# Optimization experiments

Hardware: AMD Instinct MI355X
Metric: run time of the kernel (lower is better)

The kernel has to match this reference:

```python
import jax, jax.numpy as jnp
import numpy as np

N, K, D, L = 4096, 64, 1024, 16384  # tokens, top-k, d_in, num_latents


def setup_inputs() -> dict:
    key = jax.random.key(0)
    ks = jax.random.split(key, 9)
    x = jax.random.normal(ks[0], (N, D), jnp.float32)
    y = jax.random.normal(ks[1], (N, D), jnp.float32)
    latent_acts = jax.random.uniform(ks[2], (N, K), jnp.float32)  # post-topk acts (nonneg)
    latent_indices = jax.random.randint(ks[3], (N, K), 0, L)
    W_dec = jax.random.normal(ks[4], (L, D), jnp.float32) / np.sqrt(D).astype(np.float32)
    b_dec = jax.random.normal(ks[5], (D,), jnp.float32) * 0.01
    post_enc = jax.random.normal(ks[6], (L,), jnp.float32) * 0.01
    post_enc_scale = 1.0 + 0.1 * jax.random.normal(ks[7], (L,), jnp.float32)
    W_skip = jax.random.normal(ks[8], (D, D), jnp.float32) / np.sqrt(D).astype(np.float32)
    return {
        "x": x, "y": y,
        "latent_acts": latent_acts, "latent_indices": latent_indices,
        "W_dec": W_dec, "b_dec": b_dec,
        "post_enc": post_enc, "post_enc_scale": post_enc_scale,
        "W_skip": W_skip,
    }


def reference(x, y, latent_acts, latent_indices, W_dec, b_dec, post_enc, post_enc_scale, W_skip):
    # current_latent_acts: per-index bias gather + indexed scaling
    acts = (latent_acts + post_enc[latent_indices]) * post_enc_scale[latent_indices]  # [N,K]
    # decode: gather W_dec rows by top-k indices, weighted combine, add decoder bias
    sae_out = jnp.einsum('nk,nkd->nd', acts, W_dec[latent_indices]) + b_dec  # [N,D]
    # skip connection: x @ W_skip.mT
    sae_out = sae_out + x @ W_skip.T
    # FVU loss
    e = y - sae_out
    total_variance = jnp.sum((y - jnp.mean(y, axis=0)) ** 2)
    fvu = jnp.sum(e ** 2) / total_variance
    return sae_out, fvu
```

## Files before the change

kernel.cpp:

```cpp
#include <hip/hip_runtime.h>
#include <hip/hip_bf16.h>
#include <cstdint>

#define N_TOK 4096
#define KTOP  64
#define DIM   1024
#define NLAT  16384
#define NCHUNK 8

typedef __bf16 bf16x8 __attribute__((ext_vector_type(8)));
typedef float  floatx4 __attribute__((ext_vector_type(4)));

#define GLOBAL_AS(p) ((const __attribute__((address_space(1))) void*)(p))
#define LDS_AS(p)    ((__attribute__((address_space(3))) void*)(p))

__device__ inline unsigned short f2bf(float f){
  unsigned int u = __float_as_uint(f);
  unsigned int r = (u + 0x7fffu + ((u >> 16) & 1u)) >> 16;
  return (unsigned short)r;
}
__device__ inline float bflo(unsigned int u){ return __uint_as_float(u << 16); }
__device__ inline float bfhi(unsigned int u){ return __uint_as_float(u & 0xffff0000u); }

__global__ __launch_bounds__(256) void cvt_bf16_kernel(
    const float* __restrict__ in, unsigned short* __restrict__ out, int n4){
  int i = blockIdx.x * blockDim.x + threadIdx.x;
  if (i >= n4) return;
  float4 v = ((const float4*)in)[i];
  ushort4 o;
  o.x = f2bf(v.x); o.y = f2bf(v.y); o.z = f2bf(v.z); o.w = f2bf(v.w);
  ((ushort4*)out)[i] = o;
}

__global__ __launch_bounds__(256) void cvt_wdec_chunked(
    const float* __restrict__ Wd, unsigned short* __restrict__ out){
  const int lat = blockIdx.x;
  const int t   = threadIdx.x;
  float4 v = ((const float4*)(Wd + (size_t)lat * DIM))[t];
  ushort4 o;
  o.x = f2bf(v.x); o.y = f2bf(v.y); o.z = f2bf(v.z); o.w = f2bf(v.w);
  const int chunk = t >> 5;
  const int off   = (t & 31) * 4;
  *(ushort4*)(out + ((size_t)chunk * NLAT + lat) * 128 + off) = o;
}

__global__ __launch_bounds__(256) void skip_gemm(
    const unsigned short* __restrict__ xb,
    const unsigned short* __restrict__ wb,
    const float* __restrict__ b_dec,
    float* __restrict__ out){
  __shared__ unsigned short As[128][32];
  __shared__ unsigned short Bs[128][32];
  const int row0 = blockIdx.x * 128;
  const int col0 = blockIdx.y * 128;
  const int t    = threadIdx.x;
  const int lane = t & 63;
  const int w    = t >> 6;
  const int wr   = (w >> 1) * 64;
  const int wc   = (w & 1) * 64;
  const int lm   = lane & 15;
  const int kq   = lane >> 4;
  const int sr   = t >> 2;
  const int sc   = (t & 3) * 8;

  floatx4 acc[4][4] = {};

  for (int k0 = 0; k0 < DIM; k0 += 32){
    __builtin_amdgcn_global_load_lds(GLOBAL_AS(xb + (size_t)(row0 + sr) * DIM + k0 + sc),
                                     LDS_AS(&As[sr][sc]), 16, 0, 0);
    __builtin_amdgcn_global_load_lds(GLOBAL_AS(xb + (size_t)(row0 + 64 + sr) * DIM + k0 + sc),
                                     LDS_AS(&As[64 + sr][sc]), 16, 0, 0);
    __builtin_amdgcn_global_load_lds(GLOBAL_AS(wb + (size_t)(col0 + sr) * DIM + k0 + sc),
                                     LDS_AS(&Bs[sr][sc]), 16, 0, 0);
    __builtin_amdgcn_global_load_lds(GLOBAL_AS(wb + (size_t)(col0 + 64 + sr) * DIM + k0 + sc),
                                     LDS_AS(&Bs[64 + sr][sc]), 16, 0, 0);
    __syncthreads();
    bf16x8 af[4], bfr[4];
    #pragma unroll
    for (int mi = 0; mi < 4; mi++) af[mi] = *(const bf16x8*)(&As[wr + mi * 16 + lm][kq * 8]);
    #pragma unroll
    for (int ni = 0; ni < 4; ni++) bfr[ni] = *(const bf16x8*)(&Bs[wc + ni * 16 + lm][kq * 8]);
    #pragma unroll
    for (int mi = 0; mi < 4; mi++)
      #pragma unroll
      for (int ni = 0; ni < 4; ni++)
        acc[mi][ni] = __builtin_amdgcn_mfma_f32_16x16x32_bf16(af[mi], bfr[ni], acc[mi][ni], 0, 0, 0);
    __syncthreads();
  }

  const int rq = (lane >> 4) * 4;
  #pragma unroll
  for (int mi = 0; mi < 4; mi++){
    #pragma unroll
    for (int ni = 0; ni < 4; ni++){
      int col = col0 + wc + ni * 16 + lm;
      float bd = b_dec[col];
      #pragma unroll
      for (int r = 0; r < 4; r++){
        int row = row0 + wr + mi * 16 + rq + r;
        out[(size_t)row * DIM + col] = acc[mi][ni][r] + bd;
      }
    }
  }
}

__global__ __launch_bounds__(256) void decode_residual(
    const float* __restrict__ y,
    const float* __restrict__ la,
    const int*   __restrict__ li,
    const unsigned short* __restrict__ Wdc,
    const float* __restrict__ pe,
    const float* __restrict__ pes,
    float* __restrict__ out,
    float* __restrict__ sse){
  const int chunk = blockIdx.x & 7;
  const int tok0  = (blockIdx.x >> 3) * 16;
  const int t  = threadIdx.x;
  const int tl = t >> 4;
  const int cl = t & 15;
  __shared__ float s_act[16][KTOP];
  __shared__ int   s_idx[16][KTOP];
  __shared__ float s_red[4];
  #pragma unroll
  for (int i = 0; i < 4; i++){
    int e = t + i * 256;
    int id = li[(tok0 + (e >> 6)) * KTOP + (e & 63)];
    s_idx[e >> 6][e & 63] = id;
    s_act[e >> 6][e & 63] = (la[(tok0 + (e >> 6)) * KTOP + (e & 63)] + pe[id]) * pes[id];
  }
  __syncthreads();
  const int n = tok0 + tl;
  float* op = out + (size_t)n * DIM + chunk * 128 + cl * 8;
  float4 o0 = ((const float4*)op)[0], o1 = ((const float4*)op)[1];
  float acc[8] = {o0.x, o0.y, o0.z, o0.w, o1.x, o1.y, o1.z, o1.w};
  const unsigned short* Wc = Wdc + (size_t)chunk * NLAT * 128 + cl * 8;
  #pragma unroll 8
  for (int k = 0; k < KTOP; k++){
    const float a = s_act[tl][k];
    const uint4 wv = *(const uint4*)(Wc + (size_t)s_idx[tl][k] * 128);
    acc[0] += a * bflo(wv.x); acc[1] += a * bfhi(wv.x);
    acc[2] += a * bflo(wv.y); acc[3] += a * bfhi(wv.y);
    acc[4] += a * bflo(wv.z); acc[5] += a * bfhi(wv.z);
    acc[6] += a * bflo(wv.w); acc[7] += a * bfhi(wv.w);
  }
  ((float4*)op)[0] = make_float4(acc[0], acc[1], acc[2], acc[3]);
  ((float4*)op)[1] = make_float4(acc[4], acc[5], acc[6], acc[7]);
  const float* yp = y + (size_t)n * DIM + chunk * 128 + cl * 8;
  float4 y0 = ((const float4*)yp)[0], y1 = ((const float4*)yp)[1];
  float e0 = y0.x - acc[0], e1 = y0.y - acc[1], e2 = y0.z - acc[2], e3 = y0.w - acc[3];
  float e4 = y1.x - acc[4], e5 = y1.y - acc[5], e6 = y1.z - acc[6], e7 = y1.w - acc[7];
  float s = e0*e0 + e1*e1 + e2*e2 + e3*e3 + e4*e4 + e5*e5 + e6*e6 + e7*e7;
  #pragma unroll
  for (int off = 32; off > 0; off >>= 1) s += __shfl_down(s, off, 64);
  if ((t & 63) == 0) s_red[t >> 6] = s;
  __syncthreads();
  if (t == 0) atomicAdd(sse, s_red[0] + s_red[1] + s_red[2] + s_red[3]);
}

__global__ __launch_bounds__(256) void ystats(
    const float* __restrict__ y, float* __restrict__ colsum, float* __restrict__ sumsq){
  const int t  = threadIdx.x;
  const int r0 = blockIdx.x * 32;
  float4 cs = {0.f, 0.f, 0.f, 0.f};
  float sq = 0.f;
  for (int r = 0; r < 32; r++){
    float4 v = ((const float4*)(y + (size_t)(r0 + r) * DIM))[t];
    cs.x += v.x; cs.y += v.y; cs.z += v.z; cs.w += v.w;
    sq += v.x*v.x + v.y*v.y + v.z*v.z + v.w*v.w;
  }
  atomicAdd(&colsum[t*4+0], cs.x);
  atomicAdd(&colsum[t*4+1], cs.y);
  atomicAdd(&colsum[t*4+2], cs.z);
  atomicAdd(&colsum[t*4+3], cs.w);
  #pragma unroll
  for (int off = 32; off > 0; off >>= 1) sq += __shfl_down(sq, off, 64);
  __shared__ float s_red[4];
  if ((t & 63) == 0) s_red[t >> 6] = sq;
  __syncthreads();
  if (t == 0) atomicAdd(sumsq, s_red[0] + s_red[1] + s_red[2] + s_red[3]);
}

__global__ __launch_bounds__(256) void fvu_kernel(
    const float* __restrict__ ws, float* __restrict__ fvu_out){
  const int t = threadIdx.x;
  float4 c = ((const float4*)(ws + 4))[t];
  float s = c.x*c.x + c.y*c.y + c.z*c.z + c.w*c.w;
  #pragma unroll
  for (int off = 32; off > 0; off >>= 1) s += __shfl_down(s, off, 64);
  __shared__ float s_red[4];
  if ((t & 63) == 0) s_red[t >> 6] = s;
  __syncthreads();
  if (t == 0){
    float ss = s_red[0] + s_red[1] + s_red[2] + s_red[3];
    float tv = ws[1] - ss / (float)N_TOK;
    fvu_out[0] = ws[0] / tv;
  }
}

extern "C" void kernel_launch(void* const* d_in, const int* in_sizes, int n_in,
                              void* d_out, int out_size, void* d_ws, size_t ws_size,
                              hipStream_t stream){
  const float* x   = (const float*)d_in[0];
  const float* y   = (const float*)d_in[1];
  const float* la  = (const float*)d_in[2];
  const int*   li  = (const int*)d_in[3];
  const float* Wd  = (const float*)d_in[4];
  const float* bd  = (const float*)d_in[5];
  const float* pe  = (const float*)d_in[6];
  const float* pes = (const float*)d_in[7];
  const float* Wsk = (const float*)d_in[8];
  float* out = (float*)d_out;

  float* accs = (float*)d_ws;
  unsigned short* xb  = (unsigned short*)((char*)d_ws + 8192);
  unsigned short* wb  = xb + (size_t)N_TOK * DIM;
  unsigned short* wdc = wb + (size_t)DIM * DIM;

  hipMemsetAsync(d_ws, 0, 8192, stream);
  cvt_bf16_kernel<<<N_TOK * DIM / 4 / 256, 256, 0, stream>>>(x,   xb, N_TOK * DIM / 4);
  cvt_bf16_kernel<<<DIM * DIM / 4 / 256,   256, 0, stream>>>(Wsk, wb, DIM * DIM / 4);
  cvt_wdec_chunked<<<NLAT, 256, 0, stream>>>(Wd, wdc);
  ystats<<<N_TOK / 32, 256, 0, stream>>>(y, accs + 4, accs + 1);
  skip_gemm<<<dim3(N_TOK / 128, DIM / 128), 256, 0, stream>>>(xb, wb, bd, out);
  decode_residual<<<(N_TOK / 16) * NCHUNK, 256, 0, stream>>>(y, la, li, wdc, pe, pes, out, accs);
  fvu_kernel<<<1, 256, 0, stream>>>(accs, out + (size_t)N_TOK * DIM);
}
```

Before: 242.4 us.

## Fuse prep kernels, halve skip GEMM tile width, restructure decode gather loop

```diff
diff --git a/kernel.cpp b/kernel.cpp
--- a/kernel.cpp
+++ b/kernel.cpp
@@ -22,26 +22,60 @@
 __device__ inline float bflo(unsigned int u){ return __uint_as_float(u << 16); }
 __device__ inline float bfhi(unsigned int u){ return __uint_as_float(u & 0xffff0000u); }
 
-__global__ __launch_bounds__(256) void cvt_bf16_kernel(
-    const float* __restrict__ in, unsigned short* __restrict__ out, int n4){
-  int i = blockIdx.x * blockDim.x + threadIdx.x;
-  if (i >= n4) return;
-  float4 v = ((const float4*)in)[i];
-  ushort4 o;
-  o.x = f2bf(v.x); o.y = f2bf(v.y); o.z = f2bf(v.z); o.w = f2bf(v.w);
-  ((ushort4*)out)[i] = o;
-}
-
-__global__ __launch_bounds__(256) void cvt_wdec_chunked(
-    const float* __restrict__ Wd, unsigned short* __restrict__ out){
-  const int lat = blockIdx.x;
-  const int t   = threadIdx.x;
-  float4 v = ((const float4*)(Wd + (size_t)lat * DIM))[t];
-  ushort4 o;
-  o.x = f2bf(v.x); o.y = f2bf(v.y); o.z = f2bf(v.z); o.w = f2bf(v.w);
-  const int chunk = t >> 5;
-  const int off   = (t & 31) * 4;
-  *(ushort4*)(out + ((size_t)chunk * NLAT + lat) * 128 + off) = o;
+__global__ __launch_bounds__(256) void prep(
+    const float* __restrict__ x, const float* __restrict__ Wsk,
+    const float* __restrict__ Wd, const float* __restrict__ y,
+    unsigned short* __restrict__ xb, unsigned short* __restrict__ wb,
+    unsigned short* __restrict__ wdc,
+    float* __restrict__ colsum, float* __restrict__ sumsq){
+  const int b = blockIdx.x;
+  const int t = threadIdx.x;
+  if (b < 1024){
+    int i0 = b * 1024 + t;
+    #pragma unroll
+    for (int i = 0; i < 4; i++){
+      float4 v = ((const float4*)x)[i0 + i * 256];
+      ushort4 o; o.x = f2bf(v.x); o.y = f2bf(v.y); o.z = f2bf(v.z); o.w = f2bf(v.w);
+      ((ushort4*)xb)[i0 + i * 256] = o;
+    }
+  } else if (b < 1280){
+    int i0 = (b - 1024) * 1024 + t;
+    #pragma unroll
+    for (int i = 0; i < 4; i++){
+      float4 v = ((const float4*)Wsk)[i0 + i * 256];
+      ushort4 o; o.x = f2bf(v.x); o.y = f2bf(v.y); o.z = f2bf(v.z); o.w = f2bf(v.w);
+      ((ushort4*)wb)[i0 + i * 256] = o;
+    }
+  } else if (b < 3328){
+    int lat0 = (b - 1280) * 8;
+    const int chunk = t >> 5;
+    const int off   = (t & 31) * 4;
+    for (int r = 0; r < 8; r++){
+      int lat = lat0 + r;
+      float4 v = ((const float4*)(Wd + (size_t)lat * DIM))[t];
+      ushort4 o; o.x = f2bf(v.x); o.y = f2bf(v.y); o.z = f2bf(v.z); o.w = f2bf(v.w);
+      *(ushort4*)(wdc + ((size_t)chunk * NLAT + lat) * 128 + off) = o;
+    }
+  } else {
+    const int r0 = (b - 3328) * 32;
+    float4 cs = {0.f, 0.f, 0.f, 0.f};
+    float sq = 0.f;
+    for (int r = 0; r < 32; r++){
+      float4 v = ((const float4*)(y + (size_t)(r0 + r) * DIM))[t];
+      cs.x += v.x; cs.y += v.y; cs.z += v.z; cs.w += v.w;
+      sq += v.x*v.x + v.y*v.y + v.z*v.z + v.w*v.w;
+    }
+    atomicAdd(&colsum[t*4+0], cs.x);
+    atomicAdd(&colsum[t*4+1], cs.y);
+    atomicAdd(&colsum[t*4+2], cs.z);
+    atomicAdd(&colsum[t*4+3], cs.w);
+    #pragma unroll
+    for (int off = 32; off > 0; off >>= 1) sq += __shfl_down(sq, off, 64);
+    __shared__ float s_red[4];
+    if ((t & 63) == 0) s_red[t >> 6] = sq;
+    __syncthreads();
+    if (t == 0) atomicAdd(sumsq, s_red[0] + s_red[1] + s_red[2] + s_red[3]);
+  }
 }
 
 __global__ __launch_bounds__(256) void skip_gemm(
@@ -50,20 +84,19 @@
     const float* __restrict__ b_dec,
     float* __restrict__ out){
   __shared__ unsigned short As[128][32];
-  __shared__ unsigned short Bs[128][32];
+  __shared__ unsigned short Bs[64][32];
   const int row0 = blockIdx.x * 128;
-  const int col0 = blockIdx.y * 128;
+  const int col0 = blockIdx.y * 64;
   const int t    = threadIdx.x;
   const int lane = t & 63;
   const int w    = t >> 6;
-  const int wr   = (w >> 1) * 64;
-  const int wc   = (w & 1) * 64;
+  const int wr   = w * 32;
   const int lm   = lane & 15;
   const int kq   = lane >> 4;
   const int sr   = t >> 2;
   const int sc   = (t & 3) * 8;
 
-  floatx4 acc[4][4] = {};
+  floatx4 acc[2][4] = {};
 
   for (int k0 = 0; k0 < DIM; k0 += 32){
     __builtin_amdgcn_global_load_lds(GLOBAL_AS(xb + (size_t)(row0 + sr) * DIM + k0 + sc),
@@ -72,16 +105,14 @@
                                      LDS_AS(&As[64 + sr][sc]), 16, 0, 0);
     __builtin_amdgcn_global_load_lds(GLOBAL_AS(wb + (size_t)(col0 + sr) * DIM + k0 + sc),
                                      LDS_AS(&Bs[sr][sc]), 16, 0, 0);
-    __builtin_amdgcn_global_load_lds(GLOBAL_AS(wb + (size_t)(col0 + 64 + sr) * DIM + k0 + sc),
-                                     LDS_AS(&Bs[64 + sr][sc]), 16, 0, 0);
     __syncthreads();
-    bf16x8 af[4], bfr[4];
-    #pragma unroll
-    for (int mi = 0; mi < 4; mi++) af[mi] = *(const bf16x8*)(&As[wr + mi * 16 + lm][kq * 8]);
-    #pragma unroll
-    for (int ni = 0; ni < 4; ni++) bfr[ni] = *(const bf16x8*)(&Bs[wc + ni * 16 + lm][kq * 8]);
-    #pragma unroll
-    for (int mi = 0; mi < 4; mi++)
+    bf16x8 af[2], bfr[4];
+    #pragma unroll
+    for (int mi = 0; mi < 2; mi++) af[mi] = *(const bf16x8*)(&As[wr + mi * 16 + lm][kq * 8]);
+    #pragma unroll
+    for (int ni = 0; ni < 4; ni++) bfr[ni] = *(const bf16x8*)(&Bs[ni * 16 + lm][kq * 8]);
+    #pragma unroll
+    for (int mi = 0; mi < 2; mi++)
       #pragma unroll
       for (int ni = 0; ni < 4; ni++)
         acc[mi][ni] = __builtin_amdgcn_mfma_f32_16x16x32_bf16(af[mi], bfr[ni], acc[mi][ni], 0, 0, 0);
@@ -90,10 +121,10 @@
 
   const int rq = (lane >> 4) * 4;
   #pragma unroll
-  for (int mi = 0; mi < 4; mi++){
+  for (int mi = 0; mi < 2; mi++){
     #pragma unroll
     for (int ni = 0; ni < 4; ni++){
-      int col = col0 + wc + ni * 16 + lm;
+      int col = col0 + ni * 16 + lm;
       float bd = b_dec[col];
       #pragma unroll
       for (int r = 0; r < 4; r++){
@@ -118,35 +149,38 @@
   const int t  = threadIdx.x;
   const int tl = t >> 4;
   const int cl = t & 15;
-  __shared__ float s_act[16][KTOP];
-  __shared__ int   s_idx[16][KTOP];
+  __shared__ uint2 s_ai[16][66];
   __shared__ float s_red[4];
   #pragma unroll
   for (int i = 0; i < 4; i++){
     int e = t + i * 256;
-    int id = li[(tok0 + (e >> 6)) * KTOP + (e & 63)];
-    s_idx[e >> 6][e & 63] = id;
-    s_act[e >> 6][e & 63] = (la[(tok0 + (e >> 6)) * KTOP + (e & 63)] + pe[id]) * pes[id];
+    int tok = e >> 6, k = e & 63;
+    int id = li[(tok0 + tok) * KTOP + k];
+    float a = (la[(tok0 + tok) * KTOP + k] + pe[id]) * pes[id];
+    s_ai[tok][k] = make_uint2(__float_as_uint(a), (unsigned)id * 256u);
   }
   __syncthreads();
   const int n = tok0 + tl;
+  const char* Wbase = (const char*)Wdc + (size_t)chunk * NLAT * 256 + cl * 16;
   float* op = out + (size_t)n * DIM + chunk * 128 + cl * 8;
+  const float* yp = y + (size_t)n * DIM + chunk * 128 + cl * 8;
   float4 o0 = ((const float4*)op)[0], o1 = ((const float4*)op)[1];
-  float acc[8] = {o0.x, o0.y, o0.z, o0.w, o1.x, o1.y, o1.z, o1.w};
-  const unsigned short* Wc = Wdc + (size_t)chunk * NLAT * 128 + cl * 8;
-  #pragma unroll 8
+  float4 y0 = ((const float4*)yp)[0], y1 = ((const float4*)yp)[1];
+  float acc[8] = {};
+  #pragma unroll 16
   for (int k = 0; k < KTOP; k++){
-    const float a = s_act[tl][k];
-    const uint4 wv = *(const uint4*)(Wc + (size_t)s_idx[tl][k] * 128);
+    uint2 p = s_ai[tl][k];
+    const float a = __uint_as_float(p.x);
+    const uint4 wv = *(const uint4*)(Wbase + p.y);
     acc[0] += a * bflo(wv.x); acc[1] += a * bfhi(wv.x);
     acc[2] += a * bflo(wv.y); acc[3] += a * bfhi(wv.y);
     acc[4] += a * bflo(wv.z); acc[5] += a * bfhi(wv.z);
     acc[6] += a * bflo(wv.w); acc[7] += a * bfhi(wv.w);
   }
+  acc[0] += o0.x; acc[1] += o0.y; acc[2] += o0.z; acc[3] += o0.w;
+  acc[4] += o1.x; acc[5] += o1.y; acc[6] += o1.z; acc[7] += o1.w;
   ((float4*)op)[0] = make_float4(acc[0], acc[1], acc[2], acc[3]);
   ((float4*)op)[1] = make_float4(acc[4], acc[5], acc[6], acc[7]);
-  const float* yp = y + (size_t)n * DIM + chunk * 128 + cl * 8;
-  float4 y0 = ((const float4*)yp)[0], y1 = ((const float4*)yp)[1];
   float e0 = y0.x - acc[0], e1 = y0.y - acc[1], e2 = y0.z - acc[2], e3 = y0.w - acc[3];
   float e4 = y1.x - acc[4], e5 = y1.y - acc[5], e6 = y1.z - acc[6], e7 = y1.w - acc[7];
   float s = e0*e0 + e1*e1 + e2*e2 + e3*e3 + e4*e4 + e5*e5 + e6*e6 + e7*e7;
@@ -155,29 +189,6 @@
   if ((t & 63) == 0) s_red[t >> 6] = s;
   __syncthreads();
   if (t == 0) atomicAdd(sse, s_red[0] + s_red[1] + s_red[2] + s_red[3]);
-}
-
-__global__ __launch_bounds__(256) void ystats(
-    const float* __restrict__ y, float* __restrict__ colsum, float* __restrict__ sumsq){
-  const int t  = threadIdx.x;
-  const int r0 = blockIdx.x * 32;
-  float4 cs = {0.f, 0.f, 0.f, 0.f};
-  float sq = 0.f;
-  for (int r = 0; r < 32; r++){
-    float4 v = ((const float4*)(y + (size_t)(r0 + r) * DIM))[t];
-    cs.x += v.x; cs.y += v.y; cs.z += v.z; cs.w += v.w;
-    sq += v.x*v.x + v.y*v.y + v.z*v.z + v.w*v.w;
-  }
-  atomicAdd(&colsum[t*4+0], cs.x);
-  atomicAdd(&colsum[t*4+1], cs.y);
-  atomicAdd(&colsum[t*4+2], cs.z);
-  atomicAdd(&colsum[t*4+3], cs.w);
-  #pragma unroll
-  for (int off = 32; off > 0; off >>= 1) sq += __shfl_down(sq, off, 64);
-  __shared__ float s_red[4];
-  if ((t & 63) == 0) s_red[t >> 6] = sq;
-  __syncthreads();
-  if (t == 0) atomicAdd(sumsq, s_red[0] + s_red[1] + s_red[2] + s_red[3]);
 }
 
 __global__ __launch_bounds__(256) void fvu_kernel(
@@ -217,11 +228,8 @@
   unsigned short* wdc = wb + (size_t)DIM * DIM;
 
   hipMemsetAsync(d_ws, 0, 8192, stream);
-  cvt_bf16_kernel<<<N_TOK * DIM / 4 / 256, 256, 0, stream>>>(x,   xb, N_TOK * DIM / 4);
-  cvt_bf16_kernel<<<DIM * DIM / 4 / 256,   256, 0, stream>>>(Wsk, wb, DIM * DIM / 4);
-  cvt_wdec_chunked<<<NLAT, 256, 0, stream>>>(Wd, wdc);
-  ystats<<<N_TOK / 32, 256, 0, stream>>>(y, accs + 4, accs + 1);
-  skip_gemm<<<dim3(N_TOK / 128, DIM / 128), 256, 0, stream>>>(xb, wb, bd, out);
+  prep<<<3456, 256, 0, stream>>>(x, Wsk, Wd, y, xb, wb, wdc, accs + 4, accs + 1);
+  skip_gemm<<<dim3(N_TOK / 128, DIM / 64), 256, 0, stream>>>(xb, wb, bd, out);
   decode_residual<<<(N_TOK / 16) * NCHUNK, 256, 0, stream>>>(y, la, li, wdc, pe, pes, out, accs);
   fvu_kernel<<<1, 256, 0, stream>>>(accs, out + (size_t)N_TOK * DIM);
 }
```

After: 227.9 us. -6.0%, faster.
